# Performance work log

Hardware: AMD Instinct MI355X
Metric: run time of the kernel (lower is better)

Reference implementation:

```python
import jax, jax.numpy as jnp
import numpy as np

B, T, H, D, V = 1, 512, 12, 64, 32000  # batch, seq, heads, head_dim, vocab


def setup_inputs() -> dict:
    key = jax.random.key(0)
    k0, k1, k2, k3 = jax.random.split(key, 4)
    x = jax.random.normal(k0, (B, T, H * D), dtype=jnp.float32)
    # per-head FFN weights: torch Linear(head_dim, head_dim) -> weight (out,in)=(D,D)
    W_ffn = jax.random.normal(k1, (H, D, D), dtype=jnp.float32) * 0.02
    b_ffn = jnp.zeros((H, D), dtype=jnp.float32)
    # per-head vocab attention: torch Linear(head_dim, vocab_size, bias=False) -> weight (V,D)
    W_vocab = jax.random.normal(k2, (H, V, D), dtype=jnp.float32) * 0.02
    temps = jnp.ones((H,), dtype=jnp.float32)
    # shared vocab embedding table (vocab_size, n_embd)
    E = jax.random.normal(k3, (V, H * D), dtype=jnp.float32) * 0.02
    return {"x": x, "W_ffn": W_ffn, "b_ffn": b_ffn, "W_vocab": W_vocab,
            "temps": temps, "E": E}


def reference(x, W_ffn, b_ffn, W_vocab, temps, E):
    Bx, Tx, C = x.shape
    Hn, Dn, _ = W_ffn.shape
    xh = x.reshape(Bx, Tx, Hn, Dn)                         # (B,T,H,D)
    # per-head FFN (Linear: y = x @ W^T + b)
    ffn = jnp.einsum('bthd,hed->bthe', xh, W_ffn) + b_ffn  # (B,T,H,D)
    # per-head vocab logits against weight bank (H,V,D)
    logits = jnp.einsum('bthd,hvd->bthv', ffn, W_vocab)    # (B,T,H,V)
    temp = jnp.maximum(temps, 0.1)[None, None, :, None]    # clamp(min=0.1)
    w = jax.nn.softmax(logits / temp, axis=-1)             # (B,T,H,V)
    # back-project through per-head slices of vocab embedding table
    Eh = E.reshape(E.shape[0], Hn, Dn)                     # (V,H,D)
    out = jnp.einsum('bthv,vhd->bthd', w, Eh)              # (B,T,H,D)
    # dropout is identity at eval (p used at train only)
    return out.reshape(Bx, Tx, C)
```

## Files before the change

### kernel.cpp

```cpp
#include <hip/hip_runtime.h>
#include <hip/hip_bf16.h>
#include <cstddef>

#define T_TOK 512
#define NH    12
#define HD    64
#define NV    32000
#define CEMB  768
#define NC    50
#define VC    (NV/NC)
#define NSUB  (VC/64)
#define QTILE 256
#define LOG2E 1.44269504088896340736f

typedef short v8bf __attribute__((ext_vector_type(8)));
typedef float v4f  __attribute__((ext_vector_type(4)));

__device__ __forceinline__ unsigned short f2bf(float f) {
    unsigned u = __float_as_uint(f);
    u += 0x7fffu + ((u >> 16) & 1u);
    return (unsigned short)(u >> 16);
}
__device__ __forceinline__ unsigned cvtpk(float a, float b) {
    unsigned r;
    asm("v_cvt_pk_bf16_f32 %0, %1, %2" : "=v"(r) : "v"(a), "v"(b));
    return r;
}
__device__ __forceinline__ float bf2f(unsigned short u) {
    return __uint_as_float(((unsigned)u) << 16);
}
__device__ __forceinline__ void gld16(const void* g, void* l) {
    __builtin_amdgcn_global_load_lds(
        (const __attribute__((address_space(1))) unsigned*)g,
        (__attribute__((address_space(3))) unsigned*)l, 16, 0, 0);
}

__global__ __launch_bounds__(256) void ffn_kernel(
        const float* __restrict__ x, const float* __restrict__ Wf,
        const float* __restrict__ bf, const float* __restrict__ temps,
        unsigned short* __restrict__ Qb) {
    const int h = blockIdx.y;
    const int tl = threadIdx.x >> 6, e = threadIdx.x & 63;
    const int t = blockIdx.x * 4 + tl;
    __shared__ float xs[4][HD];
    xs[tl][e] = x[t*CEMB + h*HD + e];
    __syncthreads();
    const float4* w4  = (const float4*)(Wf + (size_t)(h*HD + e)*HD);
    const float4* xs4 = (const float4*)xs[tl];
    float acc = bf[h*HD + e];
    #pragma unroll
    for (int i = 0; i < HD/4; ++i) {
        float4 a = xs4[i], b = w4[i];
        acc += a.x*b.x + a.y*b.y + a.z*b.z + a.w*b.w;
    }
    float tau = temps[h]; tau = (tau < 0.1f) ? 0.1f : tau;
    Qb[((size_t)h*T_TOK + t)*HD + e] = f2bf(acc * LOG2E / tau);
}

__global__ __launch_bounds__(256) void e_transpose(const float* __restrict__ E,
                                                   unsigned short* __restrict__ ET) {
    const int v0 = blockIdx.x * 64, h = blockIdx.y;
    const int tid = threadIdx.x;
    __shared__ float Ts[64*65];
    #pragma unroll
    for (int r = 0; r < 4; ++r) {
        int f = tid + 256*r, v = f >> 4, d4 = f & 15;
        float4 e4 = *(const float4*)&E[(size_t)(v0 + v)*CEMB + h*HD + d4*4];
        Ts[(d4*4+0)*65 + v] = e4.x;
        Ts[(d4*4+1)*65 + v] = e4.y;
        Ts[(d4*4+2)*65 + v] = e4.z;
        Ts[(d4*4+3)*65 + v] = e4.w;
    }
    __syncthreads();
    #pragma unroll
    for (int r = 0; r < 2; ++r) {
        int u = tid + 256*r, d = u >> 3, c16 = u & 7;
        const float* row = &Ts[d*65 + c16*8];
        uint4 w;
        w.x = cvtpk(row[0], row[1]);
        w.y = cvtpk(row[2], row[3]);
        w.z = cvtpk(row[4], row[5]);
        w.w = cvtpk(row[6], row[7]);
        *(uint4*)&ET[(size_t)(h*64 + d)*NV + v0 + c16*8] = w;
    }
}

__global__ __launch_bounds__(256, 2) void flash_mfma(
        const unsigned short* __restrict__ Qb, const float* __restrict__ Wv,
        const unsigned short* __restrict__ ET, unsigned short* __restrict__ Npart,
        float* __restrict__ Zpart) {
    const int c = blockIdx.x, qg = blockIdx.y, h = blockIdx.z;
    const int tid  = threadIdx.x;
    const int wq   = tid >> 6;
    const int lane = tid & 63;
    const int l15  = lane & 15, quad = lane >> 4;
    const int X    = l15 & 7;

    __shared__ unsigned short Kb[2][64*64];
    __shared__ unsigned short Eb[2][64*64];
    __shared__ unsigned short Ps[QTILE*64];

    const int tbase = qg*QTILE + wq*64;

    v8bf qf[4][2];
    #pragma unroll
    for (int nt = 0; nt < 4; ++nt)
        #pragma unroll
        for (int kb = 0; kb < 2; ++kb)
            qf[nt][kb] = *(const v8bf*)&Qb[((size_t)h*T_TOK + tbase + nt*16 + l15)*HD
                                           + kb*32 + quad*8];

    v4f o[4][4];
    #pragma unroll
    for (int mt = 0; mt < 4; ++mt)
        #pragma unroll
        for (int nt = 0; nt < 4; ++nt) { v4f z = {0.f,0.f,0.f,0.f}; o[mt][nt] = z; }
    float zacc[4] = {0.f, 0.f, 0.f, 0.f};

    const int kv = wq*16 + (lane >> 2);
    const int Xk = kv & 7;
    const float* kgl = Wv + ((size_t)h*NV + (size_t)c*VC + kv)*HD + (lane & 3)*4;
    int kwoff[4];
    #pragma unroll
    for (int r = 0; r < 4; ++r)
        kwoff[r] = kv*64 + (((((lane&3)>>1) + 2*r) ^ Xk))*8 + (lane&1)*4;
    const int Gv = (lane & 7) ^ (lane >> 3);
    const unsigned short* eg0 = ET + (size_t)(h*64 + wq*16 + (lane >> 3))*NV
                                   + (size_t)c*VC + Gv*8;
    const unsigned short* eg1 = eg0 + (size_t)8*NV;

    {
        gld16(eg0, &Eb[0][(wq*16)*64]);
        gld16(eg1, &Eb[0][(wq*16 + 8)*64]);
        float4 k0[4];
        #pragma unroll
        for (int r = 0; r < 4; ++r) k0[r] = *(const float4*)(kgl + r*16);
        #pragma unroll
        for (int r = 0; r < 4; ++r) {
            uint2 w = { cvtpk(k0[r].x, k0[r].y), cvtpk(k0[r].z, k0[r].w) };
            *(uint2*)&Kb[0][kwoff[r]] = w;
        }
        __syncthreads();
    }

    int nb = 1;
    for (int s = 0; s < NSUB; ++s) {
        const int cur = nb ^ 1;
        const bool pre = (s + 1 < NSUB);
        float4 kr[4];
        if (pre) {
            gld16(eg0 + (s+1)*64, &Eb[nb][(wq*16)*64]);
            gld16(eg1 + (s+1)*64, &Eb[nb][(wq*16 + 8)*64]);
            #pragma unroll
            for (int r = 0; r < 4; ++r)
                kr[r] = *(const float4*)(kgl + (size_t)(s+1)*4096 + r*16);
        }

        v8bf kf[4][2];
        #pragma unroll
        for (int mt = 0; mt < 4; ++mt) {
            const int row = (mt*16 + l15)*64;
            kf[mt][0] = *(const v8bf*)&Kb[cur][row + ((quad     ^ X))*8];
            kf[mt][1] = *(const v8bf*)&Kb[cur][row + (((4+quad) ^ X))*8];
        }
        #pragma unroll
        for (int nt = 0; nt < 4; ++nt) {
            #pragma unroll
            for (int mt = 0; mt < 4; ++mt) {
                v4f sa = {0.f,0.f,0.f,0.f};
                sa = __builtin_amdgcn_mfma_f32_16x16x32_bf16(kf[mt][0], qf[nt][0], sa, 0, 0, 0);
                sa = __builtin_amdgcn_mfma_f32_16x16x32_bf16(kf[mt][1], qf[nt][1], sa, 0, 0, 0);
                float p0 = exp2f(sa[0]), p1 = exp2f(sa[1]);
                float p2 = exp2f(sa[2]), p3 = exp2f(sa[3]);
                zacc[nt] += (p0 + p1) + (p2 + p3);
                uint2 w = { cvtpk(p0, p1), cvtpk(p2, p3) };
                const int q = wq*64 + nt*16 + l15;
                *(uint2*)&Ps[q*64 + (((mt*2 + (quad>>1)) ^ X))*8 + (quad&1)*4] = w;
            }
        }

        v8bf ef[4][2];
        #pragma unroll
        for (int mt = 0; mt < 4; ++mt) {
            const int row = (mt*16 + l15)*64;
            ef[mt][0] = *(const v8bf*)&Eb[cur][row + ((quad     ^ X))*8];
            ef[mt][1] = *(const v8bf*)&Eb[cur][row + (((4+quad) ^ X))*8];
        }
        #pragma unroll
        for (int nt = 0; nt < 4; ++nt) {
            const int q = wq*64 + nt*16 + l15;
            v8bf pf0 = *(const v8bf*)&Ps[q*64 + ((quad     ^ X))*8];
            v8bf pf1 = *(const v8bf*)&Ps[q*64 + (((4+quad) ^ X))*8];
            #pragma unroll
            for (int mt = 0; mt < 4; ++mt) {
                o[mt][nt] = __builtin_amdgcn_mfma_f32_16x16x32_bf16(ef[mt][0], pf0, o[mt][nt], 0, 0, 0);
                o[mt][nt] = __builtin_amdgcn_mfma_f32_16x16x32_bf16(ef[mt][1], pf1, o[mt][nt], 0, 0, 0);
            }
        }

        if (pre) {
            #pragma unroll
            for (int r = 0; r < 4; ++r) {
                uint2 w = { cvtpk(kr[r].x, kr[r].y), cvtpk(kr[r].z, kr[r].w) };
                *(uint2*)&Kb[nb][kwoff[r]] = w;
            }
            __syncthreads();
        }
        nb ^= 1;
    }

    #pragma unroll
    for (int nt = 0; nt < 4; ++nt) {
        float z = zacc[nt];
        z += __shfl_xor(z, 16, 64);
        z += __shfl_xor(z, 32, 64);
        if (quad == 0)
            Zpart[((size_t)c*T_TOK + tbase + nt*16 + l15)*NH + h] = z;
    }
    #pragma unroll
    for (int nt = 0; nt < 4; ++nt) {
        const int t = tbase + nt*16 + l15;
        unsigned short* np = Npart + (((size_t)c*T_TOK + t)*NH + h)*HD;
        #pragma unroll
        for (int mt = 0; mt < 4; ++mt) {
            v4f ov = o[mt][nt];
            uint2 w = { cvtpk(ov[0], ov[1]), cvtpk(ov[2], ov[3]) };
            *(uint2*)&np[mt*16 + quad*4] = w;
        }
    }
}

__global__ void combine_kernel(const unsigned short* __restrict__ Npart,
                               const float* __restrict__ Zpart,
                               float* __restrict__ out) {
    const int idx = (blockIdx.x*256 + threadIdx.x)*4;
    const int t = idx / CEMB;
    const int rem = idx % CEMB;
    const int h = rem >> 6, d = rem & 63;
    float n0 = 0.f, n1 = 0.f, n2 = 0.f, n3 = 0.f, z = 0.f;
    #pragma unroll
    for (int c = 0; c < NC; ++c) {
        uint2 u = *(const uint2*)&Npart[(((size_t)c*T_TOK + t)*NH + h)*HD + d];
        n0 += bf2f((unsigned short)(u.x & 0xffffu));
        n1 += bf2f((unsigned short)(u.x >> 16));
        n2 += bf2f((unsigned short)(u.y & 0xffffu));
        n3 += bf2f((unsigned short)(u.y >> 16));
        z  += Zpart[((size_t)c*T_TOK + t)*NH + h];
    }
    const float rz = 1.0f / z;
    float4 o = { n0*rz, n1*rz, n2*rz, n3*rz };
    *(float4*)&out[idx] = o;
}

extern "C" void kernel_launch(void* const* d_in, const int* in_sizes, int n_in,
                              void* d_out, int out_size, void* d_ws, size_t ws_size,
                              hipStream_t stream) {
    const float* x     = (const float*)d_in[0];
    const float* Wf    = (const float*)d_in[1];
    const float* bf    = (const float*)d_in[2];
    const float* Wv    = (const float*)d_in[3];
    const float* temps = (const float*)d_in[4];
    const float* E     = (const float*)d_in[5];
    float* out = (float*)d_out;

    char* ws = (char*)d_ws;
    unsigned short* Npart = (unsigned short*)ws;
    float*          Zpart = (float*)(ws + 39321600);
    unsigned short* Qb    = (unsigned short*)(ws + 40550400);
    unsigned short* ET    = (unsigned short*)(ws + 41336832);

    e_transpose   <<<dim3(NV/64, NH),           256, 0, stream>>>(E, ET);
    ffn_kernel    <<<dim3(T_TOK/4, NH),         256, 0, stream>>>(x, Wf, bf, temps, Qb);
    flash_mfma    <<<dim3(NC, T_TOK/QTILE, NH), 256, 0, stream>>>(Qb, Wv, ET, Npart, Zpart);
    combine_kernel<<<dim3((T_TOK*CEMB)/1024),   256, 0, stream>>>(Npart, Zpart, out);
}
```

Baseline: 330.4 us.

## Pre-convert W_vocab to bf16 and use 512-thread blocks with async K loads

A new pass converts W_vocab to bf16 once per call, so the flash kernel can stream K tiles straight into LDS with global_load_lds instead of loading fp32, converting and storing through registers. The flash kernel now runs 8 waves of 32 tokens each per block, and the vocab split count drops from 50 to 20, which shrinks the partial-sum buffers and the combine work. MFMA sections are wrapped in s_setprio. The cost is an extra full read and write pass over W_vocab each call, plus fewer blocks in the grid (480), which may underfill the GPU.

```diff
diff --git a/kernel.cpp b/kernel.cpp
--- a/kernel.cpp
+++ b/kernel.cpp
@@ -7,7 +7,7 @@
 #define HD    64
 #define NV    32000
 #define CEMB  768
-#define NC    50
+#define NC    20
 #define VC    (NV/NC)
 #define NSUB  (VC/64)
 #define QTILE 256
@@ -33,6 +33,16 @@
     __builtin_amdgcn_global_load_lds(
         (const __attribute__((address_space(1))) unsigned*)g,
         (__attribute__((address_space(3))) unsigned*)l, 16, 0, 0);
+}
+
+__global__ __launch_bounds__(256) void wv_to_bf16(const float* __restrict__ Wv,
+                                                  unsigned short* __restrict__ Wb) {
+    const size_t i = ((size_t)blockIdx.x*256 + threadIdx.x) * 8;
+    float4 a = *(const float4*)&Wv[i];
+    float4 b = *(const float4*)&Wv[i+4];
+    uint4 w = { cvtpk(a.x, a.y), cvtpk(a.z, a.w),
+                cvtpk(b.x, b.y), cvtpk(b.z, b.w) };
+    *(uint4*)&Wb[i] = w;
 }
 
 __global__ __launch_bounds__(256) void ffn_kernel(
@@ -85,8 +95,8 @@
     }
 }
 
-__global__ __launch_bounds__(256, 2) void flash_mfma(
-        const unsigned short* __restrict__ Qb, const float* __restrict__ Wv,
+__global__ __launch_bounds__(512, 4) void flash_mfma(
+        const unsigned short* __restrict__ Qb, const unsigned short* __restrict__ Wb,
         const unsigned short* __restrict__ ET, unsigned short* __restrict__ Npart,
         float* __restrict__ Zpart) {
     const int c = blockIdx.x, qg = blockIdx.y, h = blockIdx.z;
@@ -100,60 +110,41 @@
     __shared__ unsigned short Eb[2][64*64];
     __shared__ unsigned short Ps[QTILE*64];
 
-    const int tbase = qg*QTILE + wq*64;
-
-    v8bf qf[4][2];
-    #pragma unroll
-    for (int nt = 0; nt < 4; ++nt)
+    const int tbase = qg*QTILE + wq*32;
+
+    v8bf qf[2][2];
+    #pragma unroll
+    for (int nt = 0; nt < 2; ++nt)
         #pragma unroll
         for (int kb = 0; kb < 2; ++kb)
             qf[nt][kb] = *(const v8bf*)&Qb[((size_t)h*T_TOK + tbase + nt*16 + l15)*HD
                                            + kb*32 + quad*8];
 
-    v4f o[4][4];
+    v4f o[4][2];
     #pragma unroll
     for (int mt = 0; mt < 4; ++mt)
         #pragma unroll
-        for (int nt = 0; nt < 4; ++nt) { v4f z = {0.f,0.f,0.f,0.f}; o[mt][nt] = z; }
-    float zacc[4] = {0.f, 0.f, 0.f, 0.f};
-
-    const int kv = wq*16 + (lane >> 2);
-    const int Xk = kv & 7;
-    const float* kgl = Wv + ((size_t)h*NV + (size_t)c*VC + kv)*HD + (lane & 3)*4;
-    int kwoff[4];
-    #pragma unroll
-    for (int r = 0; r < 4; ++r)
-        kwoff[r] = kv*64 + (((((lane&3)>>1) + 2*r) ^ Xk))*8 + (lane&1)*4;
-    const int Gv = (lane & 7) ^ (lane >> 3);
-    const unsigned short* eg0 = ET + (size_t)(h*64 + wq*16 + (lane >> 3))*NV
-                                   + (size_t)c*VC + Gv*8;
-    const unsigned short* eg1 = eg0 + (size_t)8*NV;
-
-    {
-        gld16(eg0, &Eb[0][(wq*16)*64]);
-        gld16(eg1, &Eb[0][(wq*16 + 8)*64]);
-        float4 k0[4];
-        #pragma unroll
-        for (int r = 0; r < 4; ++r) k0[r] = *(const float4*)(kgl + r*16);
-        #pragma unroll
-        for (int r = 0; r < 4; ++r) {
-            uint2 w = { cvtpk(k0[r].x, k0[r].y), cvtpk(k0[r].z, k0[r].w) };
-            *(uint2*)&Kb[0][kwoff[r]] = w;
-        }
-        __syncthreads();
-    }
+        for (int nt = 0; nt < 2; ++nt) { v4f z = {0.f,0.f,0.f,0.f}; o[mt][nt] = z; }
+    float zacc[2] = {0.f, 0.f};
+
+    const int rsub = lane >> 3;
+    const int Gv   = (lane & 7) ^ rsub;
+    const unsigned short* kg = Wb + ((size_t)h*NV + (size_t)c*VC + wq*8 + rsub)*HD + Gv*8;
+    const unsigned short* eg = ET + ((size_t)(h*64 + wq*8 + rsub))*NV + (size_t)c*VC + Gv*8;
+    unsigned short* kld = &Kb[0][(wq*8)*64];
+    unsigned short* eld = &Eb[0][(wq*8)*64];
+
+    gld16(kg, &Kb[0][(wq*8)*64]);
+    gld16(eg, &Eb[0][(wq*8)*64]);
+    __syncthreads();
 
     int nb = 1;
     for (int s = 0; s < NSUB; ++s) {
         const int cur = nb ^ 1;
         const bool pre = (s + 1 < NSUB);
-        float4 kr[4];
         if (pre) {
-            gld16(eg0 + (s+1)*64, &Eb[nb][(wq*16)*64]);
-            gld16(eg1 + (s+1)*64, &Eb[nb][(wq*16 + 8)*64]);
-            #pragma unroll
-            for (int r = 0; r < 4; ++r)
-                kr[r] = *(const float4*)(kgl + (size_t)(s+1)*4096 + r*16);
+            gld16(kg + (size_t)(s+1)*4096, &Kb[nb][(wq*8)*64]);
+            gld16(eg + (s+1)*64,           &Eb[nb][(wq*8)*64]);
         }
 
         v8bf kf[4][2];
@@ -164,7 +155,7 @@
             kf[mt][1] = *(const v8bf*)&Kb[cur][row + (((4+quad) ^ X))*8];
         }
         #pragma unroll
-        for (int nt = 0; nt < 4; ++nt) {
+        for (int nt = 0; nt < 2; ++nt) {
             #pragma unroll
             for (int mt = 0; mt < 4; ++mt) {
                 v4f sa = {0.f,0.f,0.f,0.f};
@@ -174,7 +165,7 @@
                 float p2 = exp2f(sa[2]), p3 = exp2f(sa[3]);
                 zacc[nt] += (p0 + p1) + (p2 + p3);
                 uint2 w = { cvtpk(p0, p1), cvtpk(p2, p3) };
-                const int q = wq*64 + nt*16 + l15;
+                const int q = wq*32 + nt*16 + l15;
                 *(uint2*)&Ps[q*64 + (((mt*2 + (quad>>1)) ^ X))*8 + (quad&1)*4] = w;
             }
         }
@@ -186,9 +177,10 @@
             ef[mt][0] = *(const v8bf*)&Eb[cur][row + ((quad     ^ X))*8];
             ef[mt][1] = *(const v8bf*)&Eb[cur][row + (((4+quad) ^ X))*8];
         }
-        #pragma unroll
-        for (int nt = 0; nt < 4; ++nt) {
-            const int q = wq*64 + nt*16 + l15;
+        __builtin_amdgcn_s_setprio(1);
+        #pragma unroll
+        for (int nt = 0; nt < 2; ++nt) {
+            const int q = wq*32 + nt*16 + l15;
             v8bf pf0 = *(const v8bf*)&Ps[q*64 + ((quad     ^ X))*8];
             v8bf pf1 = *(const v8bf*)&Ps[q*64 + (((4+quad) ^ X))*8];
             #pragma unroll
@@ -197,20 +189,14 @@
                 o[mt][nt] = __builtin_amdgcn_mfma_f32_16x16x32_bf16(ef[mt][1], pf1, o[mt][nt], 0, 0, 0);
             }
         }
-
-        if (pre) {
-            #pragma unroll
-            for (int r = 0; r < 4; ++r) {
-                uint2 w = { cvtpk(kr[r].x, kr[r].y), cvtpk(kr[r].z, kr[r].w) };
-                *(uint2*)&Kb[nb][kwoff[r]] = w;
-            }
-            __syncthreads();
-        }
+        __builtin_amdgcn_s_setprio(0);
+
+        if (pre) __syncthreads();
         nb ^= 1;
     }
 
     #pragma unroll
-    for (int nt = 0; nt < 4; ++nt) {
+    for (int nt = 0; nt < 2; ++nt) {
         float z = zacc[nt];
         z += __shfl_xor(z, 16, 64);
         z += __shfl_xor(z, 32, 64);
@@ -218,7 +204,7 @@
             Zpart[((size_t)c*T_TOK + tbase + nt*16 + l15)*NH + h] = z;
     }
     #pragma unroll
-    for (int nt = 0; nt < 4; ++nt) {
+    for (int nt = 0; nt < 2; ++nt) {
         const int t = tbase + nt*16 + l15;
         unsigned short* np = Npart + (((size_t)c*T_TOK + t)*NH + h)*HD;
         #pragma unroll
@@ -228,6 +214,7 @@
             *(uint2*)&np[mt*16 + quad*4] = w;
         }
     }
+    (void)kld; (void)eld;
 }
 
 __global__ void combine_kernel(const unsigned short* __restrict__ Npart,
@@ -265,12 +252,14 @@
 
     char* ws = (char*)d_ws;
     unsigned short* Npart = (unsigned short*)ws;
-    float*          Zpart = (float*)(ws + 39321600);
-    unsigned short* Qb    = (unsigned short*)(ws + 40550400);
-    unsigned short* ET    = (unsigned short*)(ws + 41336832);
-
+    float*          Zpart = (float*)(ws + 15728640);
+    unsigned short* Qb    = (unsigned short*)(ws + 16220160);
+    unsigned short* ET    = (unsigned short*)(ws + 17006592);
+    unsigned short* Wb    = (unsigned short*)(ws + 66158592);
+
+    wv_to_bf16    <<<dim3((NH*NV*HD)/2048),     256, 0, stream>>>(Wv, Wb);
     e_transpose   <<<dim3(NV/64, NH),           256, 0, stream>>>(E, ET);
     ffn_kernel    <<<dim3(T_TOK/4, NH),         256, 0, stream>>>(x, Wf, bf, temps, Qb);
-    flash_mfma    <<<dim3(NC, T_TOK/QTILE, NH), 256, 0, stream>>>(Qb, Wv, ET, Npart, Zpart);
+    flash_mfma    <<<dim3(NC, T_TOK/QTILE, NH), 512, 0, stream>>>(Qb, Wb, ET, Npart, Zpart);
     combine_kernel<<<dim3((T_TOK*CEMB)/1024),   256, 0, stream>>>(Npart, Zpart, out);
 }
```

Measured after the change: 391.4 us. 18.5% more time.
